# Kernel optimization log

Hardware: AMD Instinct MI355X
Metric: run time of the kernel (lower is better)

## Reference

```python
import jax, jax.numpy as jnp
import numpy as np

B, N, C, H, K = 8, 1024, 768, 12, 16


def setup_inputs() -> dict:
    key = jax.random.key(0)
    ks = jax.random.split(key, 5)
    s = 0.02
    return {
        "query": jax.random.normal(ks[0], (B, N, C), jnp.float32),
        "in_proj_weight": jax.random.normal(ks[1], (3 * C, C), jnp.float32) * s,
        "in_proj_bias": jax.random.normal(ks[2], (3 * C,), jnp.float32) * s,
        "out_proj_weight": jax.random.normal(ks[3], (C, C), jnp.float32) * s,
        "out_proj_bias": jax.random.normal(ks[4], (C,), jnp.float32) * s,
        "num_heads": H,
        "k": K,
    }


def reference(query, in_proj_weight, in_proj_bias, out_proj_weight, out_proj_bias, num_heads, k):
    b, n, c = query.shape
    hd = c // num_heads
    scale = hd ** (-0.5)
    # fused QKV projection: F.linear(x, W, b) == x @ W.T + b
    qkv = query @ in_proj_weight.T + in_proj_bias  # [B,N,3C]
    qkv = qkv.reshape(b, n, 3, num_heads, hd).transpose(2, 0, 3, 1, 4)  # [3,B,H,N,hd]
    q, kk, v = qkv[0], qkv[1], qkv[2]
    attn = jnp.einsum("bhqd,bhkd->bhqk", q, kk) * scale
    attn = jax.nn.softmax(attn, axis=-1)  # [B,H,N,N]
    kk_ = min(k, attn.shape[-1])
    vals, idx = jax.lax.top_k(attn, kk_)  # [B,H,N,k]
    bi = jnp.arange(b)[:, None, None, None]
    hi = jnp.arange(num_heads)[None, :, None, None]
    ni = jnp.arange(n)[None, None, :, None]
    topk_attn = jnp.zeros_like(attn).at[bi, hi, ni, idx].set(vals)
    den = jnp.clip(topk_attn.sum(axis=-1, keepdims=True), 1e-6, None)
    topk_attn = topk_attn / den
    out = jnp.einsum("bhqk,bhkd->bhqd", topk_attn, v)  # [B,H,N,hd]
    out = out.transpose(0, 2, 1, 3).reshape(b, n, c)
    out = out @ out_proj_weight.T + out_proj_bias
    return out, topk_attn
```

## Files before the change

### kernel.cpp

```cpp
#include <hip/hip_runtime.h>
#include <float.h>
#include <math.h>

#define B_ 8
#define N_ 1024
#define C_ 768
#define H_ 12
#define HD_ 64
#define BH_ (B_*H_)

__device__ __forceinline__ unsigned long long makekey(float v, int idx) {
    unsigned int b = __float_as_uint(v);
    unsigned int o = (b & 0x80000000u) ? ~b : (b | 0x80000000u);
    return ((unsigned long long)o << 32) | (unsigned int)(1023 - idx);
}
__device__ __forceinline__ float keyval(unsigned long long k) {
    unsigned int ordv = (unsigned int)(k >> 32);
    unsigned int fb = (ordv & 0x80000000u) ? (ordv & 0x7FFFFFFFu) : ~ordv;
    return __uint_as_float(fb);
}

template<int MM, int NN, int KD, int MODE>
__global__ void __launch_bounds__(256)
gemm_k(const float* __restrict__ A, const float* __restrict__ W,
       const float* __restrict__ bias, float* __restrict__ out)
{
    __shared__ float As[16][132];
    __shared__ float Bs[16][132];
    const int tid = threadIdx.x;
    constexpr int NBLK = NN / 128;
    const int bm = blockIdx.x / NBLK;
    const int bn = blockIdx.x % NBLK;
    const int m0 = bm * 128, n0 = bn * 128;
    const int ty = tid >> 4, tx = tid & 15;
    const int ar = tid >> 2;
    const int ac = (tid & 3) << 2;

    float acc[8][8];
#pragma unroll
    for (int i = 0; i < 8; ++i)
#pragma unroll
        for (int j = 0; j < 8; ++j) acc[i][j] = 0.f;

    const float* A0 = A + (size_t)(m0 + ar) * KD + ac;
    const float* A1 = A + (size_t)(m0 + ar + 64) * KD + ac;
    const float* W0 = W + (size_t)(n0 + ar) * KD + ac;
    const float* W1 = W + (size_t)(n0 + ar + 64) * KD + ac;

    float4 pa0 = *(const float4*)A0;
    float4 pa1 = *(const float4*)A1;
    float4 pb0 = *(const float4*)W0;
    float4 pb1 = *(const float4*)W1;

    for (int k0 = 0; k0 < KD; k0 += 16) {
        __syncthreads();
        As[ac+0][ar]    = pa0.x; As[ac+1][ar]    = pa0.y; As[ac+2][ar]    = pa0.z; As[ac+3][ar]    = pa0.w;
        As[ac+0][ar+64] = pa1.x; As[ac+1][ar+64] = pa1.y; As[ac+2][ar+64] = pa1.z; As[ac+3][ar+64] = pa1.w;
        Bs[ac+0][ar]    = pb0.x; Bs[ac+1][ar]    = pb0.y; Bs[ac+2][ar]    = pb0.z; Bs[ac+3][ar]    = pb0.w;
        Bs[ac+0][ar+64] = pb1.x; Bs[ac+1][ar+64] = pb1.y; Bs[ac+2][ar+64] = pb1.z; Bs[ac+3][ar+64] = pb1.w;
        __syncthreads();
        if (k0 + 16 < KD) {
            pa0 = *(const float4*)(A0 + k0 + 16);
            pa1 = *(const float4*)(A1 + k0 + 16);
            pb0 = *(const float4*)(W0 + k0 + 16);
            pb1 = *(const float4*)(W1 + k0 + 16);
        }
#pragma unroll
        for (int kk = 0; kk < 16; ++kk) {
            float4 a0v = *(const float4*)&As[kk][ty * 4];
            float4 a1v = *(const float4*)&As[kk][64 + ty * 4];
            float4 b0v = *(const float4*)&Bs[kk][tx * 4];
            float4 b1v = *(const float4*)&Bs[kk][64 + tx * 4];
            float av[8] = {a0v.x,a0v.y,a0v.z,a0v.w, a1v.x,a1v.y,a1v.z,a1v.w};
            float bv[8] = {b0v.x,b0v.y,b0v.z,b0v.w, b1v.x,b1v.y,b1v.z,b1v.w};
#pragma unroll
            for (int i = 0; i < 8; ++i)
#pragma unroll
                for (int j = 0; j < 8; ++j)
                    acc[i][j] = fmaf(av[i], bv[j], acc[i][j]);
        }
    }

#pragma unroll
    for (int gi = 0; gi < 2; ++gi)
#pragma unroll
    for (int i = 0; i < 4; ++i) {
        const int m = m0 + gi * 64 + ty * 4 + i;
        const int ai = gi * 4 + i;
#pragma unroll
        for (int gj = 0; gj < 2; ++gj) {
            const int o = n0 + gj * 64 + tx * 4;
            const int aj = gj * 4;
            float4 bv4 = *(const float4*)(bias + o);
            float4 v;
            v.x = acc[ai][aj+0] + bv4.x;
            v.y = acc[ai][aj+1] + bv4.y;
            v.z = acc[ai][aj+2] + bv4.z;
            v.w = acc[ai][aj+3] + bv4.w;
            if (MODE == 0) {
                *(float4*)(out + (size_t)m * NN + o) = v;
            } else {
                const int which = o / 768;
                const int r = o - which * 768;
                const int hh = r >> 6;
                const int dd = r & 63;
                const int bh = (m >> 10) * H_ + hh;
                const int nn = m & 1023;
                if (which == 1) {
                    float* dst = out + (size_t)BH_ * N_ * HD_
                               + ((size_t)bh * HD_ + dd) * N_ + nn;
                    dst[0]      = v.x;
                    dst[N_]     = v.y;
                    dst[2 * N_] = v.z;
                    dst[3 * N_] = v.w;
                } else {
                    float* dst = out + (size_t)which * ((size_t)BH_ * N_ * HD_)
                               + ((size_t)bh * N_ + nn) * HD_ + dd;
                    *(float4*)dst = v;
                }
            }
        }
    }
}

__global__ void __launch_bounds__(512, 8)
attn_k(const float* __restrict__ Qg, const float* __restrict__ Ktg,
       uint2* __restrict__ wlist)
{
    __shared__ float Qs[64][8];
    __shared__ float qm[8][64];
    __shared__ unsigned long long kbuf[8][384];
    __shared__ int cnt[8][4];
    __shared__ uint2 w16s[8][16];

    const int tid = threadIdx.x;
    const int lane = tid & 63;
    const int w = tid >> 6;
    const int rg = w >> 2;
    const int cg = w & 3;
    const int eff = (blockIdx.x & 7) * 1536 + (blockIdx.x >> 3);
    const int bh = eff >> 7;
    const int qt = eff & 127;
    const int q0 = qt << 3;
    const size_t kvbase = (size_t)bh * (N_ * HD_);

    if (tid < 128) {
        int q = tid >> 4;
        int d4 = (tid & 15) << 2;
        float4 v = *(const float4*)(Qg + kvbase + (size_t)(q0 + q) * HD_ + d4);
        Qs[d4+0][q] = v.x; Qs[d4+1][q] = v.y; Qs[d4+2][q] = v.z; Qs[d4+3][q] = v.w;
    }
    __syncthreads();

    float acc[4][4];
#pragma unroll
    for (int r = 0; r < 4; ++r)
#pragma unroll
        for (int u = 0; u < 4; ++u) acc[r][u] = 0.f;

    const int jb = (cg << 8) + (lane << 2);
    const int r0 = rg << 2;
    const float* kcol = Ktg + kvbase + jb;

#pragma unroll 8
    for (int d = 0; d < 64; ++d) {
        float4 kvv = *(const float4*)(kcol + (d << 10));
        float4 qa = *(const float4*)&Qs[d][r0];
        float qv[4] = {qa.x, qa.y, qa.z, qa.w};
#pragma unroll
        for (int r = 0; r < 4; ++r) {
            acc[r][0] = fmaf(qv[r], kvv.x, acc[r][0]);
            acc[r][1] = fmaf(qv[r], kvv.y, acc[r][1]);
            acc[r][2] = fmaf(qv[r], kvv.z, acc[r][2]);
            acc[r][3] = fmaf(qv[r], kvv.w, acc[r][3]);
        }
    }

#pragma unroll
    for (int r = 0; r < 4; ++r)
#pragma unroll
        for (int u = 0; u < 4; ++u) acc[r][u] *= 0.125f;

#pragma unroll
    for (int rr = 0; rr < 4; ++rr) {
        float lm = fmaxf(fmaxf(acc[rr][0], acc[rr][1]), fmaxf(acc[rr][2], acc[rr][3]));
        lm = fmaxf(lm, __shfl_xor(lm, 1));
        lm = fmaxf(lm, __shfl_xor(lm, 2));
        if ((lane & 3) == 0) qm[r0 + rr][(cg << 4) + (lane >> 2)] = lm;
    }
    __syncthreads();

#pragma unroll
    for (int rr = 0; rr < 4; ++rr) {
        const int r = r0 + rr;
        const int g = lane & 15;
        float sg = fmaxf(fmaxf(qm[r][g], qm[r][16 + g]),
                         fmaxf(qm[r][32 + g], qm[r][48 + g]));
        sg = fminf(sg, __shfl_xor(sg, 1));
        sg = fminf(sg, __shfl_xor(sg, 2));
        sg = fminf(sg, __shfl_xor(sg, 4));
        sg = fminf(sg, __shfl_xor(sg, 8));
        const float T = sg;
        int base = 0;
        unsigned long long lowmask = (lane == 0) ? 0ull : ((1ull << lane) - 1ull);
#pragma unroll
        for (int u = 0; u < 4; ++u) {
            bool f = acc[rr][u] >= T;
            unsigned long long m = __ballot(f);
            int pos = base + __popcll(m & lowmask);
            if (f && pos < 96) kbuf[r][cg * 96 + pos] = makekey(acc[rr][u], jb + u);
            base += __popcll(m);
        }
        if (lane == 0) cnt[r][cg] = base < 96 ? base : 96;
    }
    __syncthreads();

    {
        const int r = w;
        const int c0n = cnt[r][0], c1n = cnt[r][1], c2n = cnt[r][2], c3n = cnt[r][3];
        const int pfx1 = c0n, pfx2 = c0n + c1n, pfx3 = c0n + c1n + c2n;
        const int Ctot = pfx3 + c3n;

        auto mapk = [&](int p) -> unsigned long long {
            if (p >= Ctot) return 0ull;
            int wseg, pos;
            if (p < pfx1)      { wseg = 0; pos = p; }
            else if (p < pfx2) { wseg = 1; pos = p - pfx1; }
            else if (p < pfx3) { wseg = 2; pos = p - pfx2; }
            else               { wseg = 3; pos = p - pfx3; }
            return kbuf[r][wseg * 96 + pos];
        };

        if (Ctot <= 128) {
            unsigned long long kk0 = mapk(lane);
            unsigned long long kk1 = mapk(lane + 64);
            int n0 = 0, n1 = 0;
#pragma unroll 1
            for (int seg = 0; seg < 4; ++seg) {
                const int cn = cnt[r][seg];
                const unsigned long long* sp = &kbuf[r][seg * 96];
#pragma unroll 4
                for (int p = 0; p < cn; ++p) {
                    unsigned long long kp = sp[p];
                    n0 += (kp > kk0); n1 += (kp > kk1);
                }
            }
            float v0 = keyval(kk0), v1 = keyval(kk1);
            float mc = -FLT_MAX;
            if (n0 == 0) mc = v0;
            if (n1 == 0) mc = v1;
#pragma unroll
            for (int off = 1; off < 64; off <<= 1) mc = fmaxf(mc, __shfl_xor(mc, off));
            float e0 = (n0 < 16) ? expf(v0 - mc) : 0.f;
            float e1 = (n1 < 16) ? expf(v1 - mc) : 0.f;
            float es = e0 + e1;
#pragma unroll
            for (int off = 1; off < 64; off <<= 1) es += __shfl_xor(es, off);
            if (n0 < 16) w16s[r][n0] = make_uint2(1023u - (unsigned)(kk0 & 0xFFFFFFFFull), __float_as_uint(e0 / es));
            if (n1 < 16) w16s[r][n1] = make_uint2(1023u - (unsigned)(kk1 & 0xFFFFFFFFull), __float_as_uint(e1 / es));
        } else {
            unsigned long long kk0 = mapk(lane);
            unsigned long long kk1 = mapk(lane + 64);
            unsigned long long kk2 = mapk(lane + 128);
            unsigned long long kk3 = mapk(lane + 192);
            unsigned long long kk4 = mapk(lane + 256);
            unsigned long long kk5 = mapk(lane + 320);
            int n0 = 0, n1 = 0, n2 = 0, n3 = 0, n4 = 0, n5 = 0;
#pragma unroll 1
            for (int seg = 0; seg < 4; ++seg) {
                const int cn = cnt[r][seg];
                const unsigned long long* sp = &kbuf[r][seg * 96];
#pragma unroll 2
                for (int p = 0; p < cn; ++p) {
                    unsigned long long kp = sp[p];
                    n0 += (kp > kk0); n1 += (kp > kk1); n2 += (kp > kk2);
                    n3 += (kp > kk3); n4 += (kp > kk4); n5 += (kp > kk5);
                }
            }
            float v0 = keyval(kk0), v1 = keyval(kk1), v2 = keyval(kk2);
            float v3 = keyval(kk3), v4 = keyval(kk4), v5 = keyval(kk5);
            float mc = -FLT_MAX;
            if (n0 == 0) mc = v0;
            if (n1 == 0) mc = v1;
            if (n2 == 0) mc = v2;
            if (n3 == 0) mc = v3;
            if (n4 == 0) mc = v4;
            if (n5 == 0) mc = v5;
#pragma unroll
            for (int off = 1; off < 64; off <<= 1) mc = fmaxf(mc, __shfl_xor(mc, off));
            float e0 = (n0 < 16) ? expf(v0 - mc) : 0.f;
            float e1 = (n1 < 16) ? expf(v1 - mc) : 0.f;
            float e2 = (n2 < 16) ? expf(v2 - mc) : 0.f;
            float e3 = (n3 < 16) ? expf(v3 - mc) : 0.f;
            float e4 = (n4 < 16) ? expf(v4 - mc) : 0.f;
            float e5 = (n5 < 16) ? expf(v5 - mc) : 0.f;
            float es = e0 + e1 + e2 + e3 + e4 + e5;
#pragma unroll
            for (int off = 1; off < 64; off <<= 1) es += __shfl_xor(es, off);
            if (n0 < 16) w16s[r][n0] = make_uint2(1023u - (unsigned)(kk0 & 0xFFFFFFFFull), __float_as_uint(e0 / es));
            if (n1 < 16) w16s[r][n1] = make_uint2(1023u - (unsigned)(kk1 & 0xFFFFFFFFull), __float_as_uint(e1 / es));
            if (n2 < 16) w16s[r][n2] = make_uint2(1023u - (unsigned)(kk2 & 0xFFFFFFFFull), __float_as_uint(e2 / es));
            if (n3 < 16) w16s[r][n3] = make_uint2(1023u - (unsigned)(kk3 & 0xFFFFFFFFull), __float_as_uint(e3 / es));
            if (n4 < 16) w16s[r][n4] = make_uint2(1023u - (unsigned)(kk4 & 0xFFFFFFFFull), __float_as_uint(e4 / es));
            if (n5 < 16) w16s[r][n5] = make_uint2(1023u - (unsigned)(kk5 & 0xFFFFFFFFull), __float_as_uint(e5 / es));
        }
        asm volatile("s_waitcnt lgkmcnt(0)" ::: "memory");
        __builtin_amdgcn_sched_barrier(0);

        if (lane < 16)
            wlist[((size_t)bh * N_ + q0 + r) * 16 + lane] = w16s[r][lane];
    }
}

__global__ void __launch_bounds__(256)
pv_scatter_k(const uint2* __restrict__ wlist, const float* __restrict__ Vg,
             float* __restrict__ topk, float* __restrict__ aout)
{
    const int tid = threadIdx.x;
    const int lane = tid & 63;
    const int row = (blockIdx.x << 2) + (tid >> 6);
    const size_t base = (size_t)row << 10;
    const int bh = row >> 10;
    const int n = row & 1023;
    const int b = bh / H_;
    const int h = bh - b * H_;

    float4 z4; z4.x = z4.y = z4.z = z4.w = 0.f;
#pragma unroll
    for (int t = 0; t < 4; ++t)
        *(float4*)(topk + base + (size_t)(((t << 6) + lane) << 2)) = z4;

    const uint2* wl = wlist + (size_t)row * 16;
    const float* vb = Vg + (size_t)bh * (N_ * HD_);
    float pacc = 0.f;
#pragma unroll
    for (int t = 0; t < 16; ++t) {
        uint2 e = wl[t];
        pacc = fmaf(__uint_as_float(e.y), vb[((size_t)e.x << 6) + lane], pacc);
    }
    aout[((size_t)(b * N_ + n)) * C_ + (h << 6) + lane] = pacc;

    asm volatile("s_waitcnt vmcnt(0)" ::: "memory");
    if (lane < 16) {
        uint2 e = wl[lane];
        topk[base + e.x] = __uint_as_float(e.y);
    }
}

extern "C" void kernel_launch(void* const* d_in, const int* in_sizes, int n_in,
                              void* d_out, int out_size, void* d_ws, size_t ws_size,
                              hipStream_t stream)
{
    (void)in_sizes; (void)n_in; (void)out_size; (void)ws_size;
    const float* query = (const float*)d_in[0];
    const float* win   = (const float*)d_in[1];
    const float* bin   = (const float*)d_in[2];
    const float* wout  = (const float*)d_in[3];
    const float* bout  = (const float*)d_in[4];

    float* ws = (float*)d_ws;
    float* Qp   = ws;
    float* Ktg  = Qp  + (size_t)BH_ * N_ * HD_;
    float* Vp   = Ktg + (size_t)BH_ * N_ * HD_;
    float* aout = Vp  + (size_t)BH_ * N_ * HD_;
    uint2* wlist = (uint2*)(aout + (size_t)B_ * N_ * C_);

    float* outp = (float*)d_out;
    float* topk = outp + (size_t)B_ * N_ * C_;

    gemm_k<8192, 2304, 768, 1><<<64 * 18, 256, 0, stream>>>(query, win, bin, Qp);
    attn_k<<<BH_ * 128, 512, 0, stream>>>(Qp, Ktg, wlist);
    pv_scatter_k<<<BH_ * N_ / 4, 256, 0, stream>>>(wlist, Vp, topk, aout);
    gemm_k<8192, 768, 768, 0><<<64 * 6, 256, 0, stream>>>(aout, wout, bout, outp);
}
```

Measured before the change: 950.5 us.

## Double-buffer GEMM shared-memory tiles and remap workgroup order across XCDs

Shared-memory A/B tiles in the projection GEMM are now double-buffered, so the next tile is written into the alternate buffer after compute and only one barrier per k-step is needed instead of two. Workgroup indices are also remapped so that consecutive tiles are grouped per XCD (blockIdx & 7), which is meant to improve L2 reuse on the multi-die MI355X. This doubles LDS usage per block and assumes the tile count divides evenly by 8.

```diff
diff --git a/kernel.cpp b/kernel.cpp
--- a/kernel.cpp
+++ b/kernel.cpp
@@ -25,12 +25,14 @@
 gemm_k(const float* __restrict__ A, const float* __restrict__ W,
        const float* __restrict__ bias, float* __restrict__ out)
 {
-    __shared__ float As[16][132];
-    __shared__ float Bs[16][132];
+    __shared__ float As[2][16][132];
+    __shared__ float Bs[2][16][132];
     const int tid = threadIdx.x;
     constexpr int NBLK = NN / 128;
-    const int bm = blockIdx.x / NBLK;
-    const int bn = blockIdx.x % NBLK;
+    constexpr int NWG = (MM / 128) * NBLK;
+    const int eff = (blockIdx.x & 7) * (NWG / 8) + (blockIdx.x >> 3);
+    const int bm = eff / NBLK;
+    const int bn = eff % NBLK;
     const int m0 = bm * 128, n0 = bn * 128;
     const int ty = tid >> 4, tx = tid & 15;
     const int ar = tid >> 2;
@@ -52,25 +54,29 @@
     float4 pb0 = *(const float4*)W0;
     float4 pb1 = *(const float4*)W1;
 
+    As[0][ac+0][ar]    = pa0.x; As[0][ac+1][ar]    = pa0.y; As[0][ac+2][ar]    = pa0.z; As[0][ac+3][ar]    = pa0.w;
+    As[0][ac+0][ar+64] = pa1.x; As[0][ac+1][ar+64] = pa1.y; As[0][ac+2][ar+64] = pa1.z; As[0][ac+3][ar+64] = pa1.w;
+    Bs[0][ac+0][ar]    = pb0.x; Bs[0][ac+1][ar]    = pb0.y; Bs[0][ac+2][ar]    = pb0.z; Bs[0][ac+3][ar]    = pb0.w;
+    Bs[0][ac+0][ar+64] = pb1.x; Bs[0][ac+1][ar+64] = pb1.y; Bs[0][ac+2][ar+64] = pb1.z; Bs[0][ac+3][ar+64] = pb1.w;
+    __syncthreads();
+
+    int cur = 0;
     for (int k0 = 0; k0 < KD; k0 += 16) {
-        __syncthreads();
-        As[ac+0][ar]    = pa0.x; As[ac+1][ar]    = pa0.y; As[ac+2][ar]    = pa0.z; As[ac+3][ar]    = pa0.w;
-        As[ac+0][ar+64] = pa1.x; As[ac+1][ar+64] = pa1.y; As[ac+2][ar+64] = pa1.z; As[ac+3][ar+64] = pa1.w;
-        Bs[ac+0][ar]    = pb0.x; Bs[ac+1][ar]    = pb0.y; Bs[ac+2][ar]    = pb0.z; Bs[ac+3][ar]    = pb0.w;
-        Bs[ac+0][ar+64] = pb1.x; Bs[ac+1][ar+64] = pb1.y; Bs[ac+2][ar+64] = pb1.z; Bs[ac+3][ar+64] = pb1.w;
-        __syncthreads();
-        if (k0 + 16 < KD) {
+        const bool more = (k0 + 16 < KD);
+        if (more) {
             pa0 = *(const float4*)(A0 + k0 + 16);
             pa1 = *(const float4*)(A1 + k0 + 16);
             pb0 = *(const float4*)(W0 + k0 + 16);
             pb1 = *(const float4*)(W1 + k0 + 16);
         }
+        const float (*Ac)[132] = As[cur];
+        const float (*Bc)[132] = Bs[cur];
 #pragma unroll
         for (int kk = 0; kk < 16; ++kk) {
-            float4 a0v = *(const float4*)&As[kk][ty * 4];
-            float4 a1v = *(const float4*)&As[kk][64 + ty * 4];
-            float4 b0v = *(const float4*)&Bs[kk][tx * 4];
-            float4 b1v = *(const float4*)&Bs[kk][64 + tx * 4];
+            float4 a0v = *(const float4*)&Ac[kk][ty * 4];
+            float4 a1v = *(const float4*)&Ac[kk][64 + ty * 4];
+            float4 b0v = *(const float4*)&Bc[kk][tx * 4];
+            float4 b1v = *(const float4*)&Bc[kk][64 + tx * 4];
             float av[8] = {a0v.x,a0v.y,a0v.z,a0v.w, a1v.x,a1v.y,a1v.z,a1v.w};
             float bv[8] = {b0v.x,b0v.y,b0v.z,b0v.w, b1v.x,b1v.y,b1v.z,b1v.w};
 #pragma unroll
@@ -78,6 +84,15 @@
 #pragma unroll
                 for (int j = 0; j < 8; ++j)
                     acc[i][j] = fmaf(av[i], bv[j], acc[i][j]);
+        }
+        if (more) {
+            const int nxt = cur ^ 1;
+            As[nxt][ac+0][ar]    = pa0.x; As[nxt][ac+1][ar]    = pa0.y; As[nxt][ac+2][ar]    = pa0.z; As[nxt][ac+3][ar]    = pa0.w;
+            As[nxt][ac+0][ar+64] = pa1.x; As[nxt][ac+1][ar+64] = pa1.y; As[nxt][ac+2][ar+64] = pa1.z; As[nxt][ac+3][ar+64] = pa1.w;
+            Bs[nxt][ac+0][ar]    = pb0.x; Bs[nxt][ac+1][ar]    = pb0.y; Bs[nxt][ac+2][ar]    = pb0.z; Bs[nxt][ac+3][ar]    = pb0.w;
+            Bs[nxt][ac+0][ar+64] = pb1.x; Bs[nxt][ac+1][ar+64] = pb1.y; Bs[nxt][ac+2][ar+64] = pb1.z; Bs[nxt][ac+3][ar+64] = pb1.w;
+            __syncthreads();
+            cur = nxt;
         }
     }
 
```

Result: no change. 939.6 us (-1.1%).
